# Optimization experiments

Measured on AMD Instinct MI355X. Metric: run time of the kernel, lower is better.

## Reference

```python
import jax, jax.numpy as jnp
import numpy as np

EMBED = 128   # embed_dims
NCAM = 6      # cameras per sample
FH, FW = 6, 12  # per-camera feature map size (same at every scale here)
THRESH = 0.01   # opacity threshold (GaussianRenderer.threshold)
SIZES = [25, 50, 100, 200]  # int(200 * 2**(s - 4 + 1)) for s in 0..3


def setup_inputs() -> dict:
    key = jax.random.key(0)
    ks = jax.random.split(key, 16)
    inp = {}
    for s in range(4):
        kf, km, ku, ko = ks[4 * s:4 * s + 4]
        inp[f"features{s}"] = jax.random.normal(kf, (NCAM, EMBED, FH, FW), dtype=jnp.float32)
        # means in the BEV range (-50, 50) meters
        inp[f"means{s}"] = jax.random.uniform(km, (NCAM, FH, FW, 3), minval=-50.0, maxval=50.0, dtype=jnp.float32)
        # PSD 3x3 uncertainty (covariance) per gaussian
        L = jax.random.normal(ku, (NCAM, FH, FW, 3, 3), dtype=jnp.float32)
        inp[f"uncert{s}"] = jnp.einsum('...ij,...kj->...ik', L, L) * 2.0 + jnp.eye(3, dtype=jnp.float32)
        inp[f"opac{s}"] = jax.random.uniform(ko, (NCAM, 1, FH, FW), dtype=jnp.float32)
    inp["b"] = 1
    inp["n"] = NCAM
    return inp


def _render_scale(feat, mean, unc, opac, H, W, b):
    # feat: [(b n), d, h, w]; mean: [(b n), h, w, 3]; unc: [(b n), h, w, 3, 3]; opac: [(b n), 1, h, w]
    bn, d, h, w = feat.shape
    N = (bn // b) * h * w
    f = feat.transpose(0, 2, 3, 1).reshape(b, N, d)          # b (n h w) d
    m = mean.reshape(b, N, 3)
    c9 = unc.reshape(b, N, 9)                                # flatten(-2,-1)
    # pack [xx, xy, xz, yy, yz, zz] then clamp(min=1)
    c6 = jnp.maximum(jnp.concatenate([c9[:, :, 0:3], c9[:, :, 4:6], c9[:, :, 8:9]], axis=-1), 1.0)
    o = opac.transpose(0, 2, 3, 1).reshape(b, N)

    # orthographic BEV projection: pix_row = -sh*y + H/2, pix_col = -sw*x + W/2
    sh = H / 100.0
    sw = W / 100.0
    pr = -sh * m[:, :, 1] + H / 2.0
    pc = -sw * m[:, :, 0] + W / 2.0

    # 2D covariance = J Sigma J^T with J = [[0,-sh,0],[-sw,0,0]]; +0.3 pixel dilation
    va = sh * sh * c6[:, :, 3] + 0.3   # row-row (from Sigma_yy)
    vb = sh * sw * c6[:, :, 1]         # row-col (from Sigma_xy)
    vc = sw * sw * c6[:, :, 0] + 0.3   # col-col (from Sigma_xx)
    det = va * vc - vb * vb

    rows = jnp.arange(H, dtype=feat.dtype)
    cols = jnp.arange(W, dtype=feat.dtype)
    dr = pr[:, :, None, None] - rows[None, None, :, None]    # [b,N,H,1]
    dc = pc[:, :, None, None] - cols[None, None, None, :]    # [b,N,1,W]

    power = (-0.5 * (vc[:, :, None, None] * dr * dr + va[:, :, None, None] * dc * dc)
             + vb[:, :, None, None] * dr * dc) / det[:, :, None, None]   # [b,N,H,W]

    keep = (o > THRESH) & (det > 0.0)                        # mask-gather expressed as alpha zeroing
    alpha = jnp.minimum(0.99, o[:, :, None, None] * jnp.exp(jnp.minimum(power, 0.0)))
    alpha = jnp.where(keep[:, :, None, None] & (power <= 0.0) & (alpha >= 1.0 / 255.0), alpha, 0.0)

    # front-to-back alpha compositing in gaussian order (depth is identically 0 in BEV)
    A = alpha.reshape(b, N, H * W)
    T = jnp.cumprod(1.0 - A, axis=1)
    T_excl = jnp.concatenate([jnp.ones_like(T[:, :1]), T[:, :-1]], axis=1)
    out = jnp.einsum('bnp,bnd->bdp', A * T_excl, f).reshape(b, d, H, W)  # bg color is zeros

    num_g = (o > THRESH).astype(feat.dtype).sum(1).mean()
    return out, num_g


def reference(features0, features1, features2, features3,
              means0, means1, means2, means3,
              uncert0, uncert1, uncert2, uncert3,
              opac0, opac1, opac2, opac3, b, n):
    feats = [features0, features1, features2, features3]
    means = [means0, means1, means2, means3]
    uncs = [uncert0, uncert1, uncert2, uncert3]
    ops = [opac0, opac1, opac2, opac3]
    outs = []
    num_gaussians = jnp.float32(0.0)
    for s in range(4):
        o, g = _render_scale(feats[s], means[s], uncs[s], ops[s], SIZES[s], SIZES[s], b)
        outs.append(o)
        num_gaussians = num_gaussians + g
    return (outs[0], outs[1], outs[2], outs[3], num_gaussians)
```

## Files before the change

kernel.cpp:

```cpp
#include <hip/hip_runtime.h>

#define NCAM   6
#define FHW    72
#define EMBED  128
#define NG     432
#define THRESH 0.01f
#define AMIN   (1.0f/255.0f)
#define NTILES 891
#define CHUNK  32

struct Args {
    const float* feat[4];
    const float* mean[4];
    const float* unc[4];
    const float* opac[4];
    float* out;
};

__device__ __forceinline__ void tile_decode(int g, int& s, int& H, int& band, int& chunk)
{
    int tb;
    if (g < 14)       { s = 0; H = 25;  tb = g;       chunk = tb & 1;  band = tb >> 1; }
    else if (g < 66)  { s = 1; H = 50;  tb = g - 14;  chunk = tb & 3;  band = tb >> 2; }
    else if (g < 241) { s = 2; H = 100; tb = g - 66;  band = tb / 7;   chunk = tb - band * 7; }
    else              { s = 3; H = 200; tb = g - 241; band = tb / 13;  chunk = tb - band * 13; }
}

__global__ __launch_bounds__(256) void gauss_render(Args a)
{
    __shared__ float s_pr[NG], s_pc[NG], s_qa[NG], s_qb[NG], s_qc[NG], s_ok[NG];
    __shared__ unsigned short s_list[NG];
    __shared__ int s_cnt[8];
    __shared__ int s_len;
    __shared__ float s_a[2][CHUNK][64];
    __shared__ float s_f[2][CHUNK][32];

    int bb = blockIdx.x, t = threadIdx.x;

    if (bb == NTILES * 4) {
        __shared__ float red[256];
        float cnt = 0.f;
        for (int s = 0; s < 4; s++)
            for (int i = t; i < NG; i += 256)
                cnt += (a.opac[s][i] > THRESH) ? 1.f : 0.f;
        red[t] = cnt;
        __syncthreads();
        for (int st = 128; st > 0; st >>= 1) {
            if (t < st) red[t] += red[t + st];
            __syncthreads();
        }
        if (t == 0) a.out[6800000] = red[0];
        return;
    }

    int g = bb >> 2, cq = bb & 3;
    int s, H, band, chunk;
    tile_decode(g, s, H, band, chunk);
    int P = H * H;
    float* o = a.out + ((s == 0) ? 0 : (s == 1) ? 80000 : (s == 2) ? 400000 : 1680000);

    int lane = t & 63, wv = t >> 6;
    float sh = H * 0.01f;
    float r0f = (float)(band * 4), r1f = (float)min(band * 4 + 3, H - 1);
    float c0f = (float)(chunk * 16), c1f = (float)min(chunk * 16 + 15, H - 1);
    const float* mean = a.mean[s];
    const float* unc  = a.unc[s];
    const float* opac = a.opac[s];

    bool actv[2]; int rnk[2];
    #pragma unroll
    for (int p = 0; p < 2; p++) {
        int j = p * 256 + t;
        bool act = false;
        if (j < NG) {
            float m0 = mean[j*3+0], m1 = mean[j*3+1];
            float u00 = fmaxf(unc[j*9+0], 1.f);
            float u01 = fmaxf(unc[j*9+1], 1.f);
            float u11 = fmaxf(unc[j*9+4], 1.f);
            float op = opac[j];
            float pr = -sh*m1 + H*0.5f;
            float pc = -sh*m0 + H*0.5f;
            float va = sh*sh*u11 + 0.3f;
            float vb = sh*sh*u01;
            float vc = sh*sh*u00 + 0.3f;
            float det = va*vc - vb*vb;
            float qa = 0.f, qbv = 0.f, qc = 0.f, ok = 0.f;
            if (op > THRESH && det > 0.f) {
                float inv = 1.f/det;
                qa = 0.5f*vc*inv;
                qc = 0.5f*va*inv;
                qbv = vb*inv;
                ok = op;
                float thr = __logf(255.f*op);
                float Rr = sqrtf(2.f*va*thr) + 1e-2f;
                float Rc = sqrtf(2.f*vc*thr) + 1e-2f;
                act = (pr >= r0f-Rr) && (pr <= r1f+Rr) &&
                      (pc >= c0f-Rc) && (pc <= c1f+Rc);
            }
            s_pr[j]=pr; s_pc[j]=pc; s_qa[j]=qa; s_qb[j]=qbv; s_qc[j]=qc; s_ok[j]=ok;
        }
        unsigned long long m = __ballot(act);
        actv[p] = act;
        rnk[p]  = __popcll(m & ((1ull << lane) - 1ull));
        if (lane == 0) s_cnt[p*4 + wv] = __popcll(m);
    }
    __syncthreads();
    {
        int c[8];
        #pragma unroll
        for (int i = 0; i < 8; i++) c[i] = s_cnt[i];
        int pre0 = 0, pre1 = 0;
        #pragma unroll
        for (int i = 0; i < 8; i++) {
            pre0 += (i < wv) ? c[i] : 0;
            pre1 += (i < 4 + wv) ? c[i] : 0;
        }
        if (actv[0]) s_list[pre0 + rnk[0]] = (unsigned short)t;
        if (actv[1]) s_list[pre1 + rnk[1]] = (unsigned short)(256 + t);
        if (t == 0) { int tot = 0; for (int i = 0; i < 8; i++) tot += c[i]; s_len = tot; }
    }
    __syncthreads();
    int len = s_len;

    int r = lane >> 4, cc = lane & 15;
    int row = band*4 + r, col = chunk*16 + cc;
    float frow = (float)row, fcol = (float)col;
    const float* fbase = a.feat[s];
    int fk = t >> 3, fch = (t & 7) << 2;

    float acc[8];
    #pragma unroll
    for (int i = 0; i < 8; i++) acc[i] = 0.f;
    float T = 1.f;
    float4 fst = {0.f, 0.f, 0.f, 0.f};

    #define SLOAD(C0) do {                                                        \
        if (fk < min(CHUNK, len - (C0))) {                                        \
            int n_ = s_list[(C0) + fk];                                           \
            int cam_ = n_ / FHW, hw_ = n_ - cam_ * FHW;                           \
            const float* p_ = fbase + cam_ * (EMBED*FHW)                          \
                              + (cq*32 + fch) * FHW + hw_;                        \
            fst.x = p_[0]; fst.y = p_[FHW]; fst.z = p_[2*FHW]; fst.w = p_[3*FHW]; \
        } } while (0)

    #define SWRITE(C0, BUF) do {                                                  \
        int km_ = min(CHUNK, len - (C0));                                         \
        if (fk < km_)                                                             \
            *reinterpret_cast<float4*>(&s_f[BUF][fk][fch]) = fst;                 \
        _Pragma("unroll")                                                         \
        for (int i_ = 0; i_ < 8; i_++) {                                          \
            int k_ = wv*8 + i_;                                                   \
            if (k_ < km_) {                                                       \
                int n_ = s_list[(C0) + k_];                                       \
                float dr_ = s_pr[n_] - frow;                                      \
                float dc_ = s_pc[n_] - fcol;                                      \
                float pw_ = s_qb[n_]*dr_*dc_ - s_qa[n_]*dr_*dr_                   \
                            - s_qc[n_]*dc_*dc_;                                   \
                float aL_ = 0.f;                                                  \
                if (pw_ <= 0.f) {                                                 \
                    aL_ = fminf(s_ok[n_]*__expf(pw_), 0.99f);                     \
                    aL_ = (aL_ >= AMIN) ? aL_ : 0.f;                              \
                }                                                                 \
                s_a[BUF][k_][lane] = aL_;                                         \
            }                                                                     \
        } } while (0)

    if (len > 0) {
        SLOAD(0);
        SWRITE(0, 0);
        __syncthreads();
        int buf = 0;
        for (int c0 = 0; c0 < len; c0 += CHUNK) {
            bool more = (c0 + CHUNK) < len;
            if (more) SLOAD(c0 + CHUNK);
            int kmax = min(CHUNK, len - c0);
            #pragma unroll 4
            for (int k = 0; k < kmax; k++) {
                float aL = s_a[buf][k][lane];
                float w = aL * T;
                T *= (1.f - aL);
                float4 f0 = *reinterpret_cast<const float4*>(&s_f[buf][k][wv*8]);
                float4 f1 = *reinterpret_cast<const float4*>(&s_f[buf][k][wv*8 + 4]);
                acc[0] += w*f0.x; acc[1] += w*f0.y; acc[2] += w*f0.z; acc[3] += w*f0.w;
                acc[4] += w*f1.x; acc[5] += w*f1.y; acc[6] += w*f1.z; acc[7] += w*f1.w;
            }
            if (more) SWRITE(c0 + CHUNK, buf ^ 1);
            __syncthreads();
            buf ^= 1;
        }
    }
    #undef SLOAD
    #undef SWRITE

    if (row < H && col < H) {
        int pp = row*H + col;
        int choff = cq*32 + wv*8;
        #pragma unroll
        for (int i = 0; i < 8; i++)
            o[(choff + i)*P + pp] = acc[i];
    }
}

extern "C" void kernel_launch(void* const* d_in, const int* in_sizes, int n_in,
                              void* d_out, int out_size, void* d_ws, size_t ws_size,
                              hipStream_t stream)
{
    Args a;
    for (int s = 0; s < 4; s++) {
        a.feat[s] = (const float*)d_in[4 * s + 0];
        a.mean[s] = (const float*)d_in[4 * s + 1];
        a.unc[s]  = (const float*)d_in[4 * s + 2];
        a.opac[s] = (const float*)d_in[4 * s + 3];
    }
    a.out = (float*)d_out;

    gauss_render<<<NTILES * 4 + 1, 256, 0, stream>>>(a);
}
```

Before: 29.19 us.

## Use linear 64-pixel stripes with per-scale channel groups and inline alpha

Replaces the 4x16 tiles, which always used 4 fixed channel quarters, with linear 64-pixel stripes per block. Each scale gets a templated channel-group size, up to all 128 channels per block at the largest scale, so that scale launches far fewer blocks and recomputes the culling prepass far less often. Per-Gaussian parameters are compacted into shared float4/float2 arrays. Alpha is now computed inline by every wave instead of being precomputed into a shared buffer, which removes the s_a staging but makes each wave repeat the exp work. Feature staging becomes single-buffered with an extra barrier per chunk, and a stripe that spans rows culls against the full row width.

```diff
diff --git a/kernel.cpp b/kernel.cpp
--- a/kernel.cpp
+++ b/kernel.cpp
@@ -6,8 +6,7 @@
 #define NG     432
 #define THRESH 0.01f
 #define AMIN   (1.0f/255.0f)
-#define NTILES 891
-#define CHUNK  32
+#define NBLK   1139
 
 struct Args {
     const float* feat[4];
@@ -17,79 +16,55 @@
     float* out;
 };
 
-__device__ __forceinline__ void tile_decode(int g, int& s, int& H, int& band, int& chunk)
+template<int H_, int CG_>
+__device__ __forceinline__ void render_body(
+    const float* __restrict__ feat, const float* __restrict__ mean,
+    const float* __restrict__ unc,  const float* __restrict__ opac,
+    float* __restrict__ o, int stripe, int chg, int t,
+    float4* cp4, float2* cp2, int* coff, int* cnt, float* sf)
 {
-    int tb;
-    if (g < 14)       { s = 0; H = 25;  tb = g;       chunk = tb & 1;  band = tb >> 1; }
-    else if (g < 66)  { s = 1; H = 50;  tb = g - 14;  chunk = tb & 3;  band = tb >> 2; }
-    else if (g < 241) { s = 2; H = 100; tb = g - 66;  band = tb / 7;   chunk = tb - band * 7; }
-    else              { s = 3; H = 200; tb = g - 241; band = tb / 13;  chunk = tb - band * 13; }
-}
-
-__global__ __launch_bounds__(256) void gauss_render(Args a)
-{
-    __shared__ float s_pr[NG], s_pc[NG], s_qa[NG], s_qb[NG], s_qc[NG], s_ok[NG];
-    __shared__ unsigned short s_list[NG];
-    __shared__ int s_cnt[8];
-    __shared__ int s_len;
-    __shared__ float s_a[2][CHUNK][64];
-    __shared__ float s_f[2][CHUNK][32];
-
-    int bb = blockIdx.x, t = threadIdx.x;
-
-    if (bb == NTILES * 4) {
-        __shared__ float red[256];
-        float cnt = 0.f;
-        for (int s = 0; s < 4; s++)
-            for (int i = t; i < NG; i += 256)
-                cnt += (a.opac[s][i] > THRESH) ? 1.f : 0.f;
-        red[t] = cnt;
-        __syncthreads();
-        for (int st = 128; st > 0; st >>= 1) {
-            if (t < st) red[t] += red[t + st];
-            __syncthreads();
-        }
-        if (t == 0) a.out[6800000] = red[0];
-        return;
-    }
-
-    int g = bb >> 2, cq = bb & 3;
-    int s, H, band, chunk;
-    tile_decode(g, s, H, band, chunk);
-    int P = H * H;
-    float* o = a.out + ((s == 0) ? 0 : (s == 1) ? 80000 : (s == 2) ? 400000 : 1680000);
+    constexpr int P_    = H_ * H_;
+    constexpr int CHPER = CG_ / 4;
+    constexpr int CGD8  = CG_ / 8;
+    constexpr int NF4   = CGD8 / 4;
 
     int lane = t & 63, wv = t >> 6;
-    float sh = H * 0.01f;
-    float r0f = (float)(band * 4), r1f = (float)min(band * 4 + 3, H - 1);
-    float c0f = (float)(chunk * 16), c1f = (float)min(chunk * 16 + 15, H - 1);
-    const float* mean = a.mean[s];
-    const float* unc  = a.unc[s];
-    const float* opac = a.opac[s];
-
-    bool actv[2]; int rnk[2];
-    #pragma unroll
-    for (int p = 0; p < 2; p++) {
-        int j = p * 256 + t;
+    const float sh = H_ * 0.01f;
+
+    int p0 = stripe * 64;
+    int pend = min(p0 + 63, P_ - 1);
+    int r0 = p0 / H_, r1 = pend / H_;
+    float r0f = (float)r0, r1f = (float)r1;
+    float c0f, c1f;
+    if (r1 > r0) { c0f = 0.f; c1f = (float)(H_ - 1); }
+    else         { c0f = (float)(p0 - r0 * H_); c1f = (float)(pend - r0 * H_); }
+
+    float v_pr[2], v_pc[2], v_qa[2], v_qb[2], v_qc[2], v_ok[2];
+    int v_off[2], v_rnk[2];
+    bool v_act[2];
+    #pragma unroll
+    for (int pp = 0; pp < 2; pp++) {
+        int j = pp * 256 + t;
         bool act = false;
+        float pr = 0.f, pc = 0.f, qa = 0.f, qb = 0.f, qc = 0.f, ok = 0.f;
+        int off = 0;
         if (j < NG) {
             float m0 = mean[j*3+0], m1 = mean[j*3+1];
             float u00 = fmaxf(unc[j*9+0], 1.f);
             float u01 = fmaxf(unc[j*9+1], 1.f);
             float u11 = fmaxf(unc[j*9+4], 1.f);
             float op = opac[j];
-            float pr = -sh*m1 + H*0.5f;
-            float pc = -sh*m0 + H*0.5f;
+            pr = -sh*m1 + H_*0.5f;
+            pc = -sh*m0 + H_*0.5f;
             float va = sh*sh*u11 + 0.3f;
             float vb = sh*sh*u01;
             float vc = sh*sh*u00 + 0.3f;
             float det = va*vc - vb*vb;
-            float qa = 0.f, qbv = 0.f, qc = 0.f, ok = 0.f;
             if (op > THRESH && det > 0.f) {
                 float inv = 1.f/det;
                 qa = 0.5f*vc*inv;
                 qc = 0.5f*va*inv;
-                qbv = vb*inv;
+                qb = vb*inv;
                 ok = op;
                 float thr = __logf(255.f*op);
                 float Rr = sqrtf(2.f*va*thr) + 1e-2f;
@@ -97,107 +72,156 @@
                 act = (pr >= r0f-Rr) && (pr <= r1f+Rr) &&
                       (pc >= c0f-Rc) && (pc <= c1f+Rc);
             }
-            s_pr[j]=pr; s_pc[j]=pc; s_qa[j]=qa; s_qb[j]=qbv; s_qc[j]=qc; s_ok[j]=ok;
+            int cam = j / FHW;
+            off = cam * (EMBED*FHW) + (j - cam*FHW);
         }
         unsigned long long m = __ballot(act);
-        actv[p] = act;
-        rnk[p]  = __popcll(m & ((1ull << lane) - 1ull));
-        if (lane == 0) s_cnt[p*4 + wv] = __popcll(m);
+        v_act[pp] = act;
+        v_rnk[pp] = __popcll(m & ((1ull << lane) - 1ull));
+        v_pr[pp]=pr; v_pc[pp]=pc; v_qa[pp]=qa; v_qb[pp]=qb;
+        v_qc[pp]=qc; v_ok[pp]=ok; v_off[pp]=off;
+        if (lane == 0) cnt[pp*4 + wv] = __popcll(m);
     }
     __syncthreads();
-    {
-        int c[8];
+    int c8[8];
+    #pragma unroll
+    for (int i = 0; i < 8; i++) c8[i] = cnt[i];
+    int len = 0;
+    #pragma unroll
+    for (int i = 0; i < 8; i++) len += c8[i];
+    #pragma unroll
+    for (int pp = 0; pp < 2; pp++) {
+        int slot = pp*4 + wv;
+        int pre = 0;
         #pragma unroll
-        for (int i = 0; i < 8; i++) c[i] = s_cnt[i];
-        int pre0 = 0, pre1 = 0;
-        #pragma unroll
-        for (int i = 0; i < 8; i++) {
-            pre0 += (i < wv) ? c[i] : 0;
-            pre1 += (i < 4 + wv) ? c[i] : 0;
-        }
-        if (actv[0]) s_list[pre0 + rnk[0]] = (unsigned short)t;
-        if (actv[1]) s_list[pre1 + rnk[1]] = (unsigned short)(256 + t);
-        if (t == 0) { int tot = 0; for (int i = 0; i < 8; i++) tot += c[i]; s_len = tot; }
+        for (int i = 0; i < 8; i++) pre += (i < slot) ? c8[i] : 0;
+        if (v_act[pp]) {
+            int idx = pre + v_rnk[pp];
+            cp4[idx]  = make_float4(v_pr[pp], v_pc[pp], v_qa[pp], v_qb[pp]);
+            cp2[idx]  = make_float2(v_qc[pp], v_ok[pp]);
+            coff[idx] = v_off[pp];
+        }
     }
     __syncthreads();
-    int len = s_len;
-
-    int r = lane >> 4, cc = lane & 15;
-    int row = band*4 + r, col = chunk*16 + cc;
+
+    int p = p0 + lane;
+    int row = p / H_, col = p - row * H_;
     float frow = (float)row, fcol = (float)col;
-    const float* fbase = a.feat[s];
-    int fk = t >> 3, fch = (t & 7) << 2;
-
-    float acc[8];
-    #pragma unroll
-    for (int i = 0; i < 8; i++) acc[i] = 0.f;
+    int e = t >> 3, sub = t & 7;
+    int chbase = chg * CG_;
+    int wvch = wv * CHPER;
+
+    float acc[CHPER];
+    #pragma unroll
+    for (int i = 0; i < CHPER; i++) acc[i] = 0.f;
     float T = 1.f;
-    float4 fst = {0.f, 0.f, 0.f, 0.f};
-
-    #define SLOAD(C0) do {                                                        \
-        if (fk < min(CHUNK, len - (C0))) {                                        \
-            int n_ = s_list[(C0) + fk];                                           \
-            int cam_ = n_ / FHW, hw_ = n_ - cam_ * FHW;                           \
-            const float* p_ = fbase + cam_ * (EMBED*FHW)                          \
-                              + (cq*32 + fch) * FHW + hw_;                        \
-            fst.x = p_[0]; fst.y = p_[FHW]; fst.z = p_[2*FHW]; fst.w = p_[3*FHW]; \
-        } } while (0)
-
-    #define SWRITE(C0, BUF) do {                                                  \
-        int km_ = min(CHUNK, len - (C0));                                         \
-        if (fk < km_)                                                             \
-            *reinterpret_cast<float4*>(&s_f[BUF][fk][fch]) = fst;                 \
-        _Pragma("unroll")                                                         \
-        for (int i_ = 0; i_ < 8; i_++) {                                          \
-            int k_ = wv*8 + i_;                                                   \
-            if (k_ < km_) {                                                       \
-                int n_ = s_list[(C0) + k_];                                       \
-                float dr_ = s_pr[n_] - frow;                                      \
-                float dc_ = s_pc[n_] - fcol;                                      \
-                float pw_ = s_qb[n_]*dr_*dc_ - s_qa[n_]*dr_*dr_                   \
-                            - s_qc[n_]*dc_*dc_;                                   \
-                float aL_ = 0.f;                                                  \
-                if (pw_ <= 0.f) {                                                 \
-                    aL_ = fminf(s_ok[n_]*__expf(pw_), 0.99f);                     \
-                    aL_ = (aL_ >= AMIN) ? aL_ : 0.f;                              \
-                }                                                                 \
-                s_a[BUF][k_][lane] = aL_;                                         \
-            }                                                                     \
-        } } while (0)
+    float4 fst4[NF4];
+
+    auto SLOAD = [&](int c0, int kmax) {
+        if (e < kmax) {
+            const float* q = feat + coff[c0 + e] + (chbase + sub * CGD8) * FHW;
+            #pragma unroll
+            for (int i = 0; i < NF4; i++) {
+                fst4[i].x = q[(i*4+0)*FHW];
+                fst4[i].y = q[(i*4+1)*FHW];
+                fst4[i].z = q[(i*4+2)*FHW];
+                fst4[i].w = q[(i*4+3)*FHW];
+            }
+        }
+    };
+    auto SWRITE = [&](int kmax) {
+        if (e < kmax) {
+            #pragma unroll
+            for (int i = 0; i < NF4; i++)
+                *reinterpret_cast<float4*>(&sf[e*CG_ + sub*CGD8 + i*4]) = fst4[i];
+        }
+    };
 
     if (len > 0) {
-        SLOAD(0);
-        SWRITE(0, 0);
+        SLOAD(0, min(32, len));
+        SWRITE(min(32, len));
         __syncthreads();
-        int buf = 0;
-        for (int c0 = 0; c0 < len; c0 += CHUNK) {
-            bool more = (c0 + CHUNK) < len;
-            if (more) SLOAD(c0 + CHUNK);
-            int kmax = min(CHUNK, len - c0);
-            #pragma unroll 4
+        for (int c0 = 0; c0 < len; c0 += 32) {
+            int kmax = min(32, len - c0);
+            int nxt = c0 + 32;
+            bool more = nxt < len;
+            int kmn = more ? min(32, len - nxt) : 0;
+            if (more) SLOAD(nxt, kmn);
+            #pragma unroll 2
             for (int k = 0; k < kmax; k++) {
-                float aL = s_a[buf][k][lane];
+                float4 pa = cp4[c0 + k];
+                float2 pb = cp2[c0 + k];
+                float dr = pa.x - frow, dc = pa.y - fcol;
+                float pw = pa.w*dr*dc - pa.z*dr*dr - pb.x*dc*dc;
+                float aL = 0.f;
+                if (pw <= 0.f) {
+                    aL = fminf(pb.y * __expf(pw), 0.99f);
+                    aL = (aL >= AMIN) ? aL : 0.f;
+                }
                 float w = aL * T;
                 T *= (1.f - aL);
-                float4 f0 = *reinterpret_cast<const float4*>(&s_f[buf][k][wv*8]);
-                float4 f1 = *reinterpret_cast<const float4*>(&s_f[buf][k][wv*8 + 4]);
-                acc[0] += w*f0.x; acc[1] += w*f0.y; acc[2] += w*f0.z; acc[3] += w*f0.w;
-                acc[4] += w*f1.x; acc[5] += w*f1.y; acc[6] += w*f1.z; acc[7] += w*f1.w;
+                const float* frp = &sf[k*CG_ + wvch];
+                #pragma unroll
+                for (int i = 0; i < CHPER; i += 4) {
+                    float4 f = *reinterpret_cast<const float4*>(frp + i);
+                    acc[i]   += w*f.x; acc[i+1] += w*f.y;
+                    acc[i+2] += w*f.z; acc[i+3] += w*f.w;
+                }
             }
-            if (more) SWRITE(c0 + CHUNK, buf ^ 1);
             __syncthreads();
-            buf ^= 1;
-        }
-    }
-    #undef SLOAD
-    #undef SWRITE
-
-    if (row < H && col < H) {
-        int pp = row*H + col;
-        int choff = cq*32 + wv*8;
+            if (more) { SWRITE(kmn); __syncthreads(); }
+        }
+    }
+
+    if (p < P_) {
         #pragma unroll
-        for (int i = 0; i < 8; i++)
-            o[(choff + i)*P + pp] = acc[i];
+        for (int i = 0; i < CHPER; i++)
+            o[(chbase + wvch + i) * P_ + p] = acc[i];
+    }
+}
+
+__global__ __launch_bounds__(256, 4) void gauss_render(Args a)
+{
+    __shared__ float4 cp4[NG];
+    __shared__ float2 cp2[NG];
+    __shared__ int    coff[NG];
+    __shared__ int    cnt[8];
+    __shared__ __align__(16) float sf[32 * EMBED];
+
+    int bb = blockIdx.x, t = threadIdx.x;
+
+    if (bb == NBLK) {
+        __shared__ float red[256];
+        float c = 0.f;
+        for (int s = 0; s < 4; s++)
+            for (int i = t; i < NG; i += 256)
+                c += (a.opac[s][i] > THRESH) ? 1.f : 0.f;
+        red[t] = c;
+        __syncthreads();
+        for (int st = 128; st > 0; st >>= 1) {
+            if (t < st) red[t] += red[t + st];
+            __syncthreads();
+        }
+        if (t == 0) a.out[6800000] = red[0];
+        return;
+    }
+
+    if (bb < 40) {
+        int i = bb;
+        render_body<25, 32>(a.feat[0], a.mean[0], a.unc[0], a.opac[0],
+                            a.out, i >> 2, i & 3, t, cp4, cp2, coff, cnt, sf);
+    } else if (bb < 200) {
+        int i = bb - 40;
+        render_body<50, 32>(a.feat[1], a.mean[1], a.unc[1], a.opac[1],
+                            a.out + 80000, i >> 2, i & 3, t, cp4, cp2, coff, cnt, sf);
+    } else if (bb < 514) {
+        int i = bb - 200;
+        render_body<100, 64>(a.feat[2], a.mean[2], a.unc[2], a.opac[2],
+                             a.out + 400000, i >> 1, i & 1, t, cp4, cp2, coff, cnt, sf);
+    } else {
+        int i = bb - 514;
+        render_body<200, 128>(a.feat[3], a.mean[3], a.unc[3], a.opac[3],
+                              a.out + 1680000, i, 0, t, cp4, cp2, coff, cnt, sf);
     }
 }
 
@@ -214,5 +238,5 @@
     }
     a.out = (float*)d_out;
 
-    gauss_render<<<NTILES * 4 + 1, 256, 0, stream>>>(a);
+    gauss_render<<<NBLK + 1, 256, 0, stream>>>(a);
 }
```

Result: slower. 42.94 us (+47.1%).

## Split renderer into prep kernel computing per-tile weights and render kernel

Applied to the files above, without the earlier changes.

Rendering is split into two kernels. A prep kernel builds each tile's culled gaussian list once, computes the compositing weights (alpha times transmittance) with one wave per tile, writes them to workspace, and transposes features to a gaussian-major layout. The render kernel then runs a plain weighted sum over global memory with no shared-memory staging or barriers. This drops the four-fold duplicated culling and alpha work per tile. The cost is a second launch, a large workspace round-trip for the weights, and a serial one-wave pass per tile that computes every weight.

```diff
diff --git a/kernel.cpp b/kernel.cpp
--- a/kernel.cpp
+++ b/kernel.cpp
@@ -7,14 +7,13 @@
 #define THRESH 0.01f
 #define AMIN   (1.0f/255.0f)
 #define NTILES 891
-#define CHUNK  32
+#define TC     432
 
 struct Args {
     const float* feat[4];
     const float* mean[4];
     const float* unc[4];
     const float* opac[4];
-    float* out;
 };
 
 __device__ __forceinline__ void tile_decode(int g, int& s, int& H, int& band, int& chunk)
@@ -26,178 +25,177 @@
     else              { s = 3; H = 200; tb = g - 241; band = tb / 13;  chunk = tb - band * 13; }
 }
 
-__global__ __launch_bounds__(256) void gauss_render(Args a)
-{
-    __shared__ float s_pr[NG], s_pc[NG], s_qa[NG], s_qb[NG], s_qc[NG], s_ok[NG];
-    __shared__ unsigned short s_list[NG];
-    __shared__ int s_cnt[8];
-    __shared__ int s_len;
-    __shared__ float s_a[2][CHUNK][64];
-    __shared__ float s_f[2][CHUNK][32];
-
-    int bb = blockIdx.x, t = threadIdx.x;
-
-    if (bb == NTILES * 4) {
+__global__ __launch_bounds__(256) void prep(Args a, float* __restrict__ ft,
+                                            int* __restrict__ tlen,
+                                            unsigned* __restrict__ tofs,
+                                            float* __restrict__ w_ws,
+                                            float* __restrict__ out)
+{
+    int b = blockIdx.x, t = threadIdx.x;
+    if (b < NTILES) {
+        __shared__ float4 e0[TC];
+        __shared__ float4 e1[TC];
+        __shared__ int s_cnt[8];
+        int g = b;
+        int s, H, band, chunk;
+        tile_decode(g, s, H, band, chunk);
+        int lane = t & 63, wv = t >> 6;
+        float sh = H * 0.01f;
+        float r0f = (float)(band * 4), r1f = (float)min(band * 4 + 3, H - 1);
+        float c0f = (float)(chunk * 16), c1f = (float)min(chunk * 16 + 15, H - 1);
+        const float* mean = a.mean[s];
+        const float* unc  = a.unc[s];
+        const float* opac = a.opac[s];
+
+        bool v_act[2]; int v_rnk[2];
+        float v_pr[2], v_pc[2], v_qa[2], v_qb[2], v_qc[2], v_ok[2];
+        #pragma unroll
+        for (int pp = 0; pp < 2; pp++) {
+            int j = pp * 256 + t;
+            bool act = false;
+            float pr = 0.f, pc = 0.f, qa = 0.f, qb = 0.f, qc = 0.f, ok = 0.f;
+            if (j < NG) {
+                float m0 = mean[j*3+0], m1 = mean[j*3+1];
+                float u00 = fmaxf(unc[j*9+0], 1.f);
+                float u01 = fmaxf(unc[j*9+1], 1.f);
+                float u11 = fmaxf(unc[j*9+4], 1.f);
+                float op = opac[j];
+                pr = -sh*m1 + H*0.5f;
+                pc = -sh*m0 + H*0.5f;
+                float va = sh*sh*u11 + 0.3f;
+                float vb = sh*sh*u01;
+                float vc = sh*sh*u00 + 0.3f;
+                float det = va*vc - vb*vb;
+                if (op > THRESH && det > 0.f) {
+                    float inv = 1.f/det;
+                    qa = 0.5f*vc*inv;
+                    qc = 0.5f*va*inv;
+                    qb = vb*inv;
+                    ok = op;
+                    float thr = __logf(255.f*op);
+                    float Rr = sqrtf(2.f*va*thr) + 1e-2f;
+                    float Rc = sqrtf(2.f*vc*thr) + 1e-2f;
+                    act = (pr >= r0f-Rr) && (pr <= r1f+Rr) &&
+                          (pc >= c0f-Rc) && (pc <= c1f+Rc);
+                }
+            }
+            unsigned long long m = __ballot(act);
+            v_act[pp] = act;
+            v_rnk[pp] = __popcll(m & ((1ull << lane) - 1ull));
+            v_pr[pp]=pr; v_pc[pp]=pc; v_qa[pp]=qa; v_qb[pp]=qb; v_qc[pp]=qc; v_ok[pp]=ok;
+            if (lane == 0) s_cnt[pp*4 + wv] = __popcll(m);
+        }
+        __syncthreads();
+        int c8[8];
+        #pragma unroll
+        for (int i = 0; i < 8; i++) c8[i] = s_cnt[i];
+        int len = 0;
+        #pragma unroll
+        for (int i = 0; i < 8; i++) len += c8[i];
+        #pragma unroll
+        for (int pp = 0; pp < 2; pp++) {
+            int slot = pp*4 + wv;
+            int pre = 0;
+            #pragma unroll
+            for (int i = 0; i < 8; i++) pre += (i < slot) ? c8[i] : 0;
+            if (v_act[pp]) {
+                int idx = pre + v_rnk[pp];
+                e0[idx] = make_float4(v_pr[pp], v_pc[pp], v_qa[pp], v_qb[pp]);
+                e1[idx] = make_float4(v_qc[pp], v_ok[pp], 0.f, 0.f);
+                int j = pp * 256 + t;
+                tofs[g*TC + idx] = (unsigned)((s*NG + j) * EMBED);
+            }
+        }
+        if (t == 0) tlen[g] = len;
+        __syncthreads();
+
+        if (wv == 0) {
+            int row = band*4 + (lane >> 4), col = chunk*16 + (lane & 15);
+            float frow = (float)row, fcol = (float)col;
+            float T = 1.f;
+            float* wrow = w_ws + (size_t)g * (TC*64) + lane;
+            #pragma unroll 2
+            for (int k = 0; k < len; k++) {
+                float4 A = e0[k];
+                float4 B = e1[k];
+                float dr = A.x - frow, dc = A.y - fcol;
+                float pw = A.w*dr*dc - A.z*dr*dr - B.x*dc*dc;
+                float aL = 0.f;
+                if (pw <= 0.f) {
+                    aL = fminf(B.y * __expf(pw), 0.99f);
+                    aL = (aL >= AMIN) ? aL : 0.f;
+                }
+                wrow[k*64] = aL * T;
+                T *= (1.f - aL);
+            }
+        }
+    } else if (b < NTILES + 24) {
+        __shared__ float l[EMBED * 73];
+        int sc = b - NTILES;
+        int s = sc / NCAM, cam = sc - s * NCAM;
+        const float* src = a.feat[s] + cam * (EMBED * FHW);
+        for (int i = t; i < EMBED * FHW; i += 256) {
+            int d = i / FHW, hw = i - d * FHW;
+            l[d * 73 + hw] = src[i];
+        }
+        __syncthreads();
+        float* dst = ft + (s * NG + cam * FHW) * EMBED;
+        for (int e = t; e < EMBED * FHW; e += 256) {
+            int hw = e >> 7, d = e & 127;
+            dst[hw * EMBED + d] = l[d * 73 + hw];
+        }
+    } else {
         __shared__ float red[256];
-        float cnt = 0.f;
+        float c = 0.f;
         for (int s = 0; s < 4; s++)
             for (int i = t; i < NG; i += 256)
-                cnt += (a.opac[s][i] > THRESH) ? 1.f : 0.f;
-        red[t] = cnt;
+                c += (a.opac[s][i] > THRESH) ? 1.f : 0.f;
+        red[t] = c;
         __syncthreads();
         for (int st = 128; st > 0; st >>= 1) {
             if (t < st) red[t] += red[t + st];
             __syncthreads();
         }
-        if (t == 0) a.out[6800000] = red[0];
-        return;
-    }
-
-    int g = bb >> 2, cq = bb & 3;
+        if (t == 0) out[6800000] = red[0];
+    }
+}
+
+__global__ __launch_bounds__(256) void render(const float* __restrict__ ft,
+                                              const int* __restrict__ tlen,
+                                              const unsigned* __restrict__ tofs,
+                                              const float* __restrict__ w_ws,
+                                              float* __restrict__ out)
+{
+    int gb = blockIdx.x, t = threadIdx.x;
+    int g = gb >> 2, sub = gb & 3;
     int s, H, band, chunk;
     tile_decode(g, s, H, band, chunk);
     int P = H * H;
-    float* o = a.out + ((s == 0) ? 0 : (s == 1) ? 80000 : (s == 2) ? 400000 : 1680000);
-
+    float* o = out + ((s == 0) ? 0 : (s == 1) ? 80000 : (s == 2) ? 400000 : 1680000);
     int lane = t & 63, wv = t >> 6;
-    float sh = H * 0.01f;
-    float r0f = (float)(band * 4), r1f = (float)min(band * 4 + 3, H - 1);
-    float c0f = (float)(chunk * 16), c1f = (float)min(chunk * 16 + 15, H - 1);
-    const float* mean = a.mean[s];
-    const float* unc  = a.unc[s];
-    const float* opac = a.opac[s];
-
-    bool actv[2]; int rnk[2];
-    #pragma unroll
-    for (int p = 0; p < 2; p++) {
-        int j = p * 256 + t;
-        bool act = false;
-        if (j < NG) {
-            float m0 = mean[j*3+0], m1 = mean[j*3+1];
-            float u00 = fmaxf(unc[j*9+0], 1.f);
-            float u01 = fmaxf(unc[j*9+1], 1.f);
-            float u11 = fmaxf(unc[j*9+4], 1.f);
-            float op = opac[j];
-            float pr = -sh*m1 + H*0.5f;
-            float pc = -sh*m0 + H*0.5f;
-            float va = sh*sh*u11 + 0.3f;
-            float vb = sh*sh*u01;
-            float vc = sh*sh*u00 + 0.3f;
-            float det = va*vc - vb*vb;
-            float qa = 0.f, qbv = 0.f, qc = 0.f, ok = 0.f;
-            if (op > THRESH && det > 0.f) {
-                float inv = 1.f/det;
-                qa = 0.5f*vc*inv;
-                qc = 0.5f*va*inv;
-                qbv = vb*inv;
-                ok = op;
-                float thr = __logf(255.f*op);
-                float Rr = sqrtf(2.f*va*thr) + 1e-2f;
-                float Rc = sqrtf(2.f*vc*thr) + 1e-2f;
-                act = (pr >= r0f-Rr) && (pr <= r1f+Rr) &&
-                      (pc >= c0f-Rc) && (pc <= c1f+Rc);
-            }
-            s_pr[j]=pr; s_pc[j]=pc; s_qa[j]=qa; s_qb[j]=qbv; s_qc[j]=qc; s_ok[j]=ok;
-        }
-        unsigned long long m = __ballot(act);
-        actv[p] = act;
-        rnk[p]  = __popcll(m & ((1ull << lane) - 1ull));
-        if (lane == 0) s_cnt[p*4 + wv] = __popcll(m);
-    }
-    __syncthreads();
-    {
-        int c[8];
-        #pragma unroll
-        for (int i = 0; i < 8; i++) c[i] = s_cnt[i];
-        int pre0 = 0, pre1 = 0;
-        #pragma unroll
-        for (int i = 0; i < 8; i++) {
-            pre0 += (i < wv) ? c[i] : 0;
-            pre1 += (i < 4 + wv) ? c[i] : 0;
-        }
-        if (actv[0]) s_list[pre0 + rnk[0]] = (unsigned short)t;
-        if (actv[1]) s_list[pre1 + rnk[1]] = (unsigned short)(256 + t);
-        if (t == 0) { int tot = 0; for (int i = 0; i < 8; i++) tot += c[i]; s_len = tot; }
-    }
-    __syncthreads();
-    int len = s_len;
-
-    int r = lane >> 4, cc = lane & 15;
-    int row = band*4 + r, col = chunk*16 + cc;
-    float frow = (float)row, fcol = (float)col;
-    const float* fbase = a.feat[s];
-    int fk = t >> 3, fch = (t & 7) << 2;
+    int ch0 = __builtin_amdgcn_readfirstlane((sub * 4 + wv) * 8);
+    int len = tlen[g];
+    const unsigned* to = tofs + g * TC;
+    const float* wr = w_ws + (size_t)g * (TC*64) + lane;
 
     float acc[8];
     #pragma unroll
     for (int i = 0; i < 8; i++) acc[i] = 0.f;
-    float T = 1.f;
-    float4 fst = {0.f, 0.f, 0.f, 0.f};
-
-    #define SLOAD(C0) do {                                                        \
-        if (fk < min(CHUNK, len - (C0))) {                                        \
-            int n_ = s_list[(C0) + fk];                                           \
-            int cam_ = n_ / FHW, hw_ = n_ - cam_ * FHW;                           \
-            const float* p_ = fbase + cam_ * (EMBED*FHW)                          \
-                              + (cq*32 + fch) * FHW + hw_;                        \
-            fst.x = p_[0]; fst.y = p_[FHW]; fst.z = p_[2*FHW]; fst.w = p_[3*FHW]; \
-        } } while (0)
-
-    #define SWRITE(C0, BUF) do {                                                  \
-        int km_ = min(CHUNK, len - (C0));                                         \
-        if (fk < km_)                                                             \
-            *reinterpret_cast<float4*>(&s_f[BUF][fk][fch]) = fst;                 \
-        _Pragma("unroll")                                                         \
-        for (int i_ = 0; i_ < 8; i_++) {                                          \
-            int k_ = wv*8 + i_;                                                   \
-            if (k_ < km_) {                                                       \
-                int n_ = s_list[(C0) + k_];                                       \
-                float dr_ = s_pr[n_] - frow;                                      \
-                float dc_ = s_pc[n_] - fcol;                                      \
-                float pw_ = s_qb[n_]*dr_*dc_ - s_qa[n_]*dr_*dr_                   \
-                            - s_qc[n_]*dc_*dc_;                                   \
-                float aL_ = 0.f;                                                  \
-                if (pw_ <= 0.f) {                                                 \
-                    aL_ = fminf(s_ok[n_]*__expf(pw_), 0.99f);                     \
-                    aL_ = (aL_ >= AMIN) ? aL_ : 0.f;                              \
-                }                                                                 \
-                s_a[BUF][k_][lane] = aL_;                                         \
-            }                                                                     \
-        } } while (0)
-
-    if (len > 0) {
-        SLOAD(0);
-        SWRITE(0, 0);
-        __syncthreads();
-        int buf = 0;
-        for (int c0 = 0; c0 < len; c0 += CHUNK) {
-            bool more = (c0 + CHUNK) < len;
-            if (more) SLOAD(c0 + CHUNK);
-            int kmax = min(CHUNK, len - c0);
-            #pragma unroll 4
-            for (int k = 0; k < kmax; k++) {
-                float aL = s_a[buf][k][lane];
-                float w = aL * T;
-                T *= (1.f - aL);
-                float4 f0 = *reinterpret_cast<const float4*>(&s_f[buf][k][wv*8]);
-                float4 f1 = *reinterpret_cast<const float4*>(&s_f[buf][k][wv*8 + 4]);
-                acc[0] += w*f0.x; acc[1] += w*f0.y; acc[2] += w*f0.z; acc[3] += w*f0.w;
-                acc[4] += w*f1.x; acc[5] += w*f1.y; acc[6] += w*f1.z; acc[7] += w*f1.w;
-            }
-            if (more) SWRITE(c0 + CHUNK, buf ^ 1);
-            __syncthreads();
-            buf ^= 1;
-        }
-    }
-    #undef SLOAD
-    #undef SWRITE
-
+
+    #pragma unroll 4
+    for (int k = 0; k < len; k++) {
+        const float* fr = ft + to[k] + ch0;
+        float wgt = wr[k * 64];
+        #pragma unroll
+        for (int i = 0; i < 8; i++) acc[i] += wgt * fr[i];
+    }
+
+    int row = band*4 + (lane >> 4), col = chunk*16 + (lane & 15);
     if (row < H && col < H) {
-        int pp = row*H + col;
-        int choff = cq*32 + wv*8;
+        int pp = row * H + col;
         #pragma unroll
         for (int i = 0; i < 8; i++)
-            o[(choff + i)*P + pp] = acc[i];
+            o[(ch0 + i) * P + pp] = acc[i];
     }
 }
 
@@ -212,7 +210,12 @@
         a.unc[s]  = (const float*)d_in[4 * s + 2];
         a.opac[s] = (const float*)d_in[4 * s + 3];
     }
-    a.out = (float*)d_out;
-
-    gauss_render<<<NTILES * 4 + 1, 256, 0, stream>>>(a);
-}
+    float* ws = (float*)d_ws;
+    float*    ft    = ws;
+    int*      tlen  = (int*)(ws + 221184);
+    unsigned* tofs  = (unsigned*)(ws + 222080);
+    float*    w_ws  = ws + 700000;
+
+    prep<<<NTILES + 24 + 1, 256, 0, stream>>>(a, ft, tlen, tofs, w_ws, (float*)d_out);
+    render<<<NTILES * 4, 256, 0, stream>>>(ft, tlen, tofs, w_ws, (float*)d_out);
+}
```

Result: slower. 36.97 us (+26.7%).
